# Kernel tuning notes

Hardware: AMD Instinct MI355X
Metric: run time of the kernel (lower is better)

Reference implementation:

```python
import jax, jax.numpy as jnp
import numpy as np

B = 32          # patients
D = 128         # hidden dim (modality_embedding_dim == total_hidden_dim)
H = 4           # attention heads
DH = D // H     # per-head dim
L = 2           # num_graph_layers
N = {'ct': 1024, 'pet': 1024, 'clin': 256, 'gen': 2048, 'pat': 1}
# (src_type, dst_type) for the 8 relation types registered in _setup_relations
REL = [('ct','ct'), ('pet','pet'), ('clin','clin'), ('gen','gen'),
       ('pat','clin'), ('ct','gen'), ('pet','gen'), ('gen','pat')]
E_REL = [8192, 8192, 2048, 16384, 256, 8192, 8192, 2048]
EDGE_NAMES = ['e_ct','e_pet','e_clin','e_gen','e_pat2clin','e_ct2gen','e_pet2gen','e_gen2pat']


def setup_inputs() -> dict:
    key = jax.random.key(0)
    ks = iter(jax.random.split(key, 64))
    nk = lambda: next(ks)
    inp = {}
    inp['x_ct']   = jax.random.normal(nk(), (B, N['ct'],  D), jnp.float32)
    inp['x_pet']  = jax.random.normal(nk(), (B, N['pet'], D), jnp.float32)
    inp['x_clin'] = jax.random.normal(nk(), (B, N['clin'],D), jnp.float32)
    inp['x_gen']  = jax.random.normal(nk(), (B, N['gen'], D), jnp.float32)
    inp['early']  = jax.random.normal(nk(), (B, D), jnp.float32)

    def mk_edges(k, E, ns, nd):
        k1, k2 = jax.random.split(k)
        src = jax.random.randint(k1, (B, 1, E), 0, ns, jnp.int32)
        dst = jax.random.randint(k2, (B, 1, E), 0, nd, jnp.int32)
        return jnp.concatenate([src, dst], axis=1)  # [B,2,E]

    for nm, (s, d), E in zip(EDGE_NAMES, REL, E_REL):
        inp[nm] = mk_edges(nk(), E, N[s], N[d])

    sw = 1.0 / np.sqrt(D)
    inp['W_src'] = jax.random.normal(nk(), (L, 8, D, D), jnp.float32) * sw
    inp['W_dst'] = jax.random.normal(nk(), (L, 8, D, D), jnp.float32) * sw
    inp['a_src'] = jax.random.normal(nk(), (L, 8, H, DH), jnp.float32) * sw
    inp['a_dst'] = jax.random.normal(nk(), (L, 8, H, DH), jnp.float32) * sw
    inp['Wp'] = jax.random.normal(nk(), (3, D, D), jnp.float32) * sw  # CT, PET, genomic pooling
    inp['bp'] = jnp.zeros((3, D), jnp.float32)
    inp['W_sem'] = jax.random.normal(nk(), (4 * D, 128), jnp.float32) * (1.0 / np.sqrt(4 * D))
    inp['b_sem'] = jnp.zeros((128,), jnp.float32)
    inp['q_sem'] = jax.random.normal(nk(), (128,), jnp.float32) * sw
    return inp


def _leaky_relu(x):
    return jnp.where(x > 0, x, 0.2 * x)


def _gat_layer(x, edges, Ws, Wd, As, Ad):
    """One heterogeneous multi-head GAT layer summing over relation types."""
    agg = {t: jnp.zeros((B, N[t], H, DH), jnp.float32) for t in N}
    for r, ((s, d), ei) in enumerate(zip(REL, edges)):
        hs = jnp.einsum('bnd,de->bne', x[s], Ws[r]).reshape(B, N[s], H, DH)
        hd = jnp.einsum('bnd,de->bne', x[d], Wd[r]).reshape(B, N[d], H, DH)
        al_s = jnp.sum(hs * As[r], axis=-1)  # [B,Ns,H]
        al_d = jnp.sum(hd * Ad[r], axis=-1)  # [B,Nd,H]
        nd = N[d]

        def one(hs_b, as_b, ad_b, e_b):
            src, dst = e_b[0], e_b[1]
            logit = _leaky_relu(as_b[src] + ad_b[dst])                      # [E,H]
            m = jnp.full((nd, H), -1e30, logit.dtype).at[dst].max(logit)    # segment max
            p = jnp.exp(logit - m[dst])
            den = jnp.zeros((nd, H), p.dtype).at[dst].add(p)
            w = p / (den[dst] + 1e-16)                                      # edge softmax per dst node
            msg = w[:, :, None] * hs_b[src]                                 # [E,H,DH]
            return jnp.zeros((nd, H, DH), msg.dtype).at[dst].add(msg)

        agg[d] = agg[d] + jax.vmap(one)(hs, al_s, al_d, ei)
    return {t: jax.nn.elu(agg[t].reshape(B, N[t], D)) for t in N}


def _pool(feat, W, b):
    # query = Linear(mean(features)); scores = feat @ q; softmax-weighted sum
    q = jnp.mean(feat, axis=1) @ W + b            # [B,D]
    sc = jnp.einsum('bnd,bd->bn', feat, q)        # [B,N]
    w = jax.nn.softmax(sc, axis=1)
    return jnp.einsum('bn,bnd->bd', w, feat)      # [B,D]


def _forward(x_ct, x_pet, x_clin, x_gen, early, edges,
             W_src, W_dst, a_src, a_dst, Wp, bp, W_sem, b_sem, q_sem):
    x = {'ct': x_ct, 'pet': x_pet, 'clin': x_clin, 'gen': x_gen,
         'pat': early[:, None, :]}
    for l in range(L):
        x = _gat_layer(x, edges, W_src[l], W_dst[l], a_src[l], a_dst[l])
    ct_p  = _pool(x['ct'],  Wp[0], bp[0])
    pet_p = _pool(x['pet'], Wp[1], bp[1])
    gen_p = _pool(x['gen'], Wp[2], bp[2])   # shared across the 3 meta-paths
    pad = jnp.zeros((B, 2 * D), ct_p.dtype)  # pad 2D -> 4D as in original
    imm = jnp.concatenate([ct_p, gen_p, pad], axis=1)
    pro = jnp.concatenate([pet_p, gen_p, pad], axis=1)
    trt = jnp.concatenate([(ct_p + pet_p) * 0.5, gen_p, pad], axis=1)
    z = jnp.stack([imm, pro, trt], axis=1)                     # [B,3,4D]
    s = jnp.einsum('bpa,a->bp', jnp.tanh(jnp.einsum('bpf,fa->bpa', z, W_sem) + b_sem), q_sem)
    beta = jax.nn.softmax(s, axis=1)                           # [B,3]
    fused = jnp.einsum('bp,bpf->bf', beta, z)                  # [B,4D]
    return fused, beta


def reference(x_ct, x_pet, x_clin, x_gen, early,
              e_ct, e_pet, e_clin, e_gen, e_pat2clin, e_ct2gen, e_pet2gen, e_gen2pat,
              W_src, W_dst, a_src, a_dst, Wp, bp, W_sem, b_sem, q_sem):
    edges = [e_ct, e_pet, e_clin, e_gen, e_pat2clin, e_ct2gen, e_pet2gen, e_gen2pat]
    return _forward(x_ct, x_pet, x_clin, x_gen, early, edges,
                    W_src, W_dst, a_src, a_dst, Wp, bp, W_sem, b_sem, q_sem)
```

## Files before the change

kernel.cpp:

```cpp
#include <hip/hip_runtime.h>
#include <math.h>

static constexpr int NB = 32;
static constexpr int ND = 128;

typedef short bf16x8 __attribute__((ext_vector_type(8)));
typedef float f32x4  __attribute__((ext_vector_type(4)));
typedef unsigned short u16x8 __attribute__((ext_vector_type(8)));

__device__ __forceinline__ float lrelu(float x){ return x > 0.f ? x : 0.2f*x; }
__device__ __forceinline__ unsigned short f2b(float f){
  unsigned u = __float_as_uint(f);
  return (unsigned short)((u + 0x7FFFu + ((u>>16)&1u)) >> 16);
}
__device__ __forceinline__ float b2f(unsigned short b){
  return __uint_as_float(((unsigned)b) << 16);
}

__global__ __launch_bounds__(128) void k_fold(const float* __restrict__ Wsrc,
    const float* __restrict__ Wdst, const float* __restrict__ asrc,
    const float* __restrict__ adst, float* __restrict__ vbuf){
  const int wid[5] = {0,1,3,5,6};
  int lr = blockIdx.x, role = blockIdx.y, l = blockIdx.z;
  int r = wid[lr];
  const float* W = (role ? Wdst : Wsrc) + (size_t)(l*8+r)*16384;
  const float* a = (role ? adst : asrc) + (size_t)(l*8+r)*128;
  int k = threadIdx.x;
  float* o = vbuf + ((size_t)((l*5+lr)*2+role))*512 + k*4;
  #pragma unroll
  for(int h=0;h<4;h++){
    float s = 0.f;
    #pragma unroll
    for(int j=0;j<32;j++) s += W[k*128 + h*32 + j]*a[h*32 + j];
    o[h] = s;
  }
}

__global__ __launch_bounds__(256) void k_wpack(const float* __restrict__ Wsrc,
    unsigned short* __restrict__ Wf){
  const int wid[5] = {0,1,3,5,6};
  int lr = blockIdx.x, l = blockIdx.y;
  const float* W = Wsrc + (size_t)(l*8+wid[lr])*16384;
  unsigned short* o = Wf + (size_t)((l*5+lr)*4)*4096;
  for(int idx=threadIdx.x; idx<128*128; idx+=256){
    int k = idx >> 7, col = idx & 127;
    int h = col >> 5, cc = col & 31;
    int k4 = k>>2, g = k4&3, kk = k4>>3, j = 4*((k4>>2)&1) + (k&3);
    int nb = cc>>4, lane = (cc&15) + 16*g;
    o[(size_t)h*4096 + ((size_t)((kk*2+nb)*64 + lane))*8 + j] = f2b(W[k*128 + col]);
  }
}

struct CsrP {
  const int* eg[5];
  int l2E[5];
  int Nd_[5];
  int roff_[5];
  int eoff_[5];
};

__global__ __launch_bounds__(512) void k_csr(CsrP P, int* __restrict__ rowstart,
                                             int* __restrict__ srcidx){
  int b = blockIdx.x, r = blockIdx.y, t = threadIdx.x;
  int E = 1<<P.l2E[r], Nd = P.Nd_[r];
  const int* eg = P.eg[r] + (size_t)b*2*E;
  int* rsO = rowstart + P.roff_[r] + b*(Nd+1);
  int* siO = srcidx + P.eoff_[r] + (size_t)b*E;
  __shared__ int cnt[2048];
  __shared__ int wsums[8];
  for(int i=t;i<Nd;i+=512) cnt[i]=0;
  __syncthreads();
  for(int e=t;e<E;e+=512) atomicAdd(&cnt[eg[E+e]], 1);
  __syncthreads();
  int C = Nd >> 9;
  int base = t*C;
  int loc[4]; int s_=0;
  for(int i=0;i<C;i++){ loc[i]=cnt[base+i]; s_+=loc[i]; }
  int lane = t&63, wv = t>>6;
  int sinc = s_;
  #pragma unroll
  for(int off=1;off<64;off<<=1){
    int u = __shfl_up(sinc, off);
    if(lane>=off) sinc += u;
  }
  if(lane==63) wsums[wv]=sinc;
  __syncthreads();
  int wbase=0, total=0;
  #pragma unroll
  for(int i=0;i<8;i++){ int v=wsums[i]; if(i<wv) wbase+=v; total+=v; }
  int excl = wbase + sinc - s_;
  for(int i=0;i<C;i++){
    int idx=base+i;
    rsO[idx]=excl; cnt[idx]=excl; excl+=loc[i];
  }
  if(t==0) rsO[Nd]=total;
  __syncthreads();
  for(int e=t;e<E;e+=512){
    int src=eg[e], dst=eg[E+e];
    int pos=atomicAdd(&cnt[dst],1);
    siO[pos]=src;
  }
}

struct HsP {
  int tb[4];
  int usef;
  const float* xf[3];
  unsigned long long xoff[3];
  int Ns[3];
  int nW[3];
  unsigned long long wfo[3][2];
  unsigned long long hso[3][2];
  unsigned long long aso[3][2];
  unsigned long long asrco[3][2];
  int nvd[3];
  unsigned long long vdo[3][3];
  unsigned long long aldo2[3][3];
  int ndd[3][3];
};

__global__ __launch_bounds__(256) void k_hs(HsP P, const unsigned short* __restrict__ x16,
    const unsigned short* __restrict__ Wf, const float* __restrict__ asrc,
    const float* __restrict__ vbuf, unsigned short* __restrict__ hs,
    float* __restrict__ als, float* __restrict__ ald){
  __shared__ unsigned short xl[32*132];
  __shared__ unsigned short obuf[32*136];
  int B = blockIdx.x;
  int t=0; while(t<2 && B>=P.tb[t+1]) t++;
  int local = B - P.tb[t];
  int b = local & 31, tile = local >> 5;
  int n0 = tile*32;
  int tid = threadIdx.x, w = tid>>6, ln = tid&63;
  {
    int row = tid>>3, c16 = (tid&7)*16;
    if(P.usef){
      const float* xf = P.xf[t] + ((size_t)((size_t)b*P.Ns[t] + n0 + row))*128 + c16;
      #pragma unroll
      for(int half=0; half<2; half++){
        float4 a = *(const float4*)(xf + half*8);
        float4 c = *(const float4*)(xf + half*8 + 4);
        u16x8 r;
        r[0]=f2b(a.x); r[1]=f2b(a.y); r[2]=f2b(a.z); r[3]=f2b(a.w);
        r[4]=f2b(c.x); r[5]=f2b(c.y); r[6]=f2b(c.z); r[7]=f2b(c.w);
        *(u16x8*)&xl[row*132 + c16 + half*8] = r;
      }
    } else {
      const unsigned short* xb = x16 + P.xoff[t] + ((size_t)((size_t)b*P.Ns[t] + n0 + row))*128 + c16;
      u16x8 v0 = *(const u16x8*)xb;
      u16x8 v1 = *(const u16x8*)(xb + 8);
      *(u16x8*)&xl[row*132 + c16]     = v0;
      *(u16x8*)&xl[row*132 + c16 + 8] = v1;
    }
  }
  __syncthreads();
  int g = ln>>4, r15 = ln&15;
  for(int rep=0; rep<P.nW[t]; rep++){
    const unsigned short* wf = Wf + P.wfo[t][rep] + (size_t)w*4096;
    bf16x8 bw[8];
    #pragma unroll
    for(int kk=0;kk<4;kk++){
      #pragma unroll
      for(int nb=0;nb<2;nb++)
        bw[kk*2+nb] = *(const bf16x8*)(wf + ((size_t)((kk*2+nb)*64 + ln))*8);
    }
    const float* aS = asrc + P.asrco[t][rep];
    float a0v = aS[w*32 + r15], a1v = aS[w*32 + 16 + r15];
    #pragma unroll
    for(int c=0;c<2;c++){
      f32x4 acc[2]; acc[0]=(f32x4){0,0,0,0}; acc[1]=(f32x4){0,0,0,0};
      #pragma unroll
      for(int kk=0;kk<4;kk++){
        const unsigned short* pa = &xl[(c*16 + r15)*132 + kk*32 + 4*g];
        ushort4 lo = *(const ushort4*)pa;
        ushort4 hi = *(const ushort4*)(pa+16);
        union { ushort u[8]; bf16x8 v; } tmp;
        tmp.u[0]=lo.x; tmp.u[1]=lo.y; tmp.u[2]=lo.z; tmp.u[3]=lo.w;
        tmp.u[4]=hi.x; tmp.u[5]=hi.y; tmp.u[6]=hi.z; tmp.u[7]=hi.w;
        bf16x8 af = tmp.v;
        acc[0] = __builtin_amdgcn_mfma_f32_16x16x32_bf16(af, bw[kk*2+0], acc[0], 0, 0, 0);
        acc[1] = __builtin_amdgcn_mfma_f32_16x16x32_bf16(af, bw[kk*2+1], acc[1], 0, 0, 0);
      }
      #pragma unroll
      for(int qq=0;qq<4;qq++){
        int m = c*16 + 4*g + qq;
        obuf[m*136 + w*32 + r15]      = f2b(acc[0][qq]);
        obuf[m*136 + w*32 + 16 + r15] = f2b(acc[1][qq]);
      }
      float p0 = acc[0][0]*a0v + acc[1][0]*a1v;
      float p1 = acc[0][1]*a0v + acc[1][1]*a1v;
      float p2 = acc[0][2]*a0v + acc[1][2]*a1v;
      float p3 = acc[0][3]*a0v + acc[1][3]*a1v;
      #pragma unroll
      for(int off=1; off<16; off<<=1){
        p0 += __shfl_xor(p0,off); p1 += __shfl_xor(p1,off);
        p2 += __shfl_xor(p2,off); p3 += __shfl_xor(p3,off);
      }
      if(r15 < 4){
        float pv = (r15==0)?p0:((r15==1)?p1:((r15==2)?p2:p3));
        als[P.aso[t][rep] + ((size_t)b*P.Ns[t] + n0 + c*16 + 4*g + r15)*4 + w] = pv;
      }
    }
    __syncthreads();
    {
      unsigned short* ho = hs + P.hso[t][rep] + ((size_t)b*P.Ns[t] + n0)*128;
      int row = tid>>3, c16 = (tid&7)*16;
      u16x8 o0 = *(const u16x8*)&obuf[row*136 + c16];
      u16x8 o1 = *(const u16x8*)&obuf[row*136 + c16 + 8];
      *(u16x8*)(ho + (size_t)row*128 + c16)     = o0;
      *(u16x8*)(ho + (size_t)row*128 + c16 + 8) = o1;
    }
    __syncthreads();
  }
  int nvd = P.nvd[t];
  for(int s=tid; s<(nvd<<7); s+=256){
    int vd = s>>7, rem = s&127, row = rem>>2, h = rem&3;
    const float* vv = vbuf + P.vdo[t][vd];
    float sum = 0.f;
    #pragma unroll 8
    for(int k=0;k<128;k++) sum += b2f(xl[row*132+k]) * vv[k*4+h];
    ald[P.aldo2[t][vd] + ((size_t)b*P.ndd[t][vd] + n0 + row)*4 + h] = sum;
  }
}

static constexpr int WSL = 240;

struct Fu5P {
  int nrel[3], ndshift[3];
  int roff[3][3], eoff[3][3], E[3][3], Ns[3][3];
  int rowbase[3][3];
  unsigned long long aldo[3][3];
  unsigned long long outoff[3];
};

__global__ __launch_bounds__(512, 8) void k_fuse7(Fu5P P,
    const int* __restrict__ rowstart, const int* __restrict__ srcidx,
    const float* __restrict__ als, const float* __restrict__ ald,
    const unsigned short* __restrict__ hs, unsigned short* __restrict__ out16){
  __shared__ float wlds_all[8*4*WSL];
  __shared__ int   silds_all[8*WSL];
  int B = blockIdx.x;
  int w = threadIdx.x >> 6, ln = threadIdx.x & 63;
  int xcd = B & 7, slot = B >> 3;
  int bg = slot >> 6, rem = slot & 63;
  int b = bg*8 + xcd;
  int v = rem*8 + w;
  int g = v >> 2, k4 = v & 3;
  int t, tile;
  if(k4 < 2){ t = 0; tile = g*2 + k4; }
  else if(k4 == 2){ t = 1; tile = g; }
  else { t = 2; tile = g; }
  int Nd = 1 << P.ndshift[t];
  int d0 = tile * 8;
  int nrel = P.nrel[t];
  float* wlds = wlds_all + w*4*WSL;
  int*  silds = silds_all + w*WSL;
  int dst = ln >> 3, sub = ln & 7;
  int d = d0 + dst;

  int len0=0, len1=0, len2=0, s00=0, s01=0, s02=0;
  {
    const int* rsq = rowstart + P.roff[t][0] + b*(Nd+1);
    s00 = rsq[d]; len0 = rsq[d+1] - s00;
  }
  if(nrel > 1){
    const int* rsq1 = rowstart + P.roff[t][1] + b*(Nd+1);
    s01 = rsq1[d]; len1 = rsq1[d+1] - s01;
    const int* rsq2 = rowstart + P.roff[t][2] + b*(Nd+1);
    s02 = rsq2[d]; len2 = rsq2[d+1] - s02;
  }
  int clen = len0 + len1 + len2;
  int mybase = 0;
  #pragma unroll
  for(int dd=0; dd<7; dd++){
    int vl = __shfl(clen, dd*8);
    if(dd < dst) mybase += vl;
  }

  auto dorel = [&](int q, int s0q, int lq, int segb){
    const int* si = srcidx + P.eoff[t][q] + (size_t)b*P.E[t][q] + s0q;
    int bake = P.rowbase[t][q] + b*P.Ns[t][q];
    float4 ad4 = *(const float4*)(ald + P.aldo[t][q] + ((size_t)b*Nd + d)*4);
    float dn0=0.f, dn1=0.f, dn2=0.f, dn3=0.f;
    for(int i=sub; i<lq; i+=8){
      int e = segb + i;
      int sil = bake + si[i];
      silds[e] = sil;
      float4 as4 = *(const float4*)(als + 4*(size_t)sil);
      float p0 = __expf(lrelu(as4.x+ad4.x));
      float p1 = __expf(lrelu(as4.y+ad4.y));
      float p2 = __expf(lrelu(as4.z+ad4.z));
      float p3 = __expf(lrelu(as4.w+ad4.w));
      wlds[0*WSL+e]=p0; wlds[1*WSL+e]=p1; wlds[2*WSL+e]=p2; wlds[3*WSL+e]=p3;
      dn0+=p0; dn1+=p1; dn2+=p2; dn3+=p3;
    }
    dn0+=__shfl_xor(dn0,1); dn1+=__shfl_xor(dn1,1); dn2+=__shfl_xor(dn2,1); dn3+=__shfl_xor(dn3,1);
    dn0+=__shfl_xor(dn0,2); dn1+=__shfl_xor(dn1,2); dn2+=__shfl_xor(dn2,2); dn3+=__shfl_xor(dn3,2);
    dn0+=__shfl_xor(dn0,4); dn1+=__shfl_xor(dn1,4); dn2+=__shfl_xor(dn2,4); dn3+=__shfl_xor(dn3,4);
    float i0=1.f/(dn0+1e-16f), i1=1.f/(dn1+1e-16f);
    float i2=1.f/(dn2+1e-16f), i3=1.f/(dn3+1e-16f);
    for(int i=sub; i<lq; i+=8){
      int e = segb + i;
      wlds[0*WSL+e]*=i0; wlds[1*WSL+e]*=i1;
      wlds[2*WSL+e]*=i2; wlds[3*WSL+e]*=i3;
    }
  };
  dorel(0, s00, len0, mybase);
  if(nrel > 1){
    dorel(1, s01, len1, mybase + len0);
    dorel(2, s02, len2, mybase + len0 + len1);
  }
  __builtin_amdgcn_wave_barrier();

  int h = ln>>4;
  int run = 0;
  #pragma unroll
  for(int it=0; it<8; it++){
    int cl = __shfl(clen, it*8);
    int e0 = run, e1 = run + cl; run = e1;
    float a0 = 0.f, a1 = 0.f;
    int e = e0;
    int eal = (e0+3)&~3; if(eal > e1) eal = e1;
    for(; e<eal; e++){
      float wv = wlds[h*WSL + e];
      unsigned vv = *(const unsigned*)(hs + ((size_t)silds[e]*128 + 2*ln));
      a0 += wv*__uint_as_float(vv<<16);
      a1 += wv*__uint_as_float(vv&0xFFFF0000u);
    }
    for(; e+8<=e1; e+=8){
      int4  sq0 = *(const int4*)&silds[e];
      int4  sq1 = *(const int4*)&silds[e+4];
      float4 wq0 = *(const float4*)&wlds[h*WSL + e];
      float4 wq1 = *(const float4*)&wlds[h*WSL + e + 4];
      unsigned v0 = *(const unsigned*)(hs + ((size_t)sq0.x*128 + 2*ln));
      unsigned v1 = *(const unsigned*)(hs + ((size_t)sq0.y*128 + 2*ln));
      unsigned v2 = *(const unsigned*)(hs + ((size_t)sq0.z*128 + 2*ln));
      unsigned v3 = *(const unsigned*)(hs + ((size_t)sq0.w*128 + 2*ln));
      unsigned v4 = *(const unsigned*)(hs + ((size_t)sq1.x*128 + 2*ln));
      unsigned v5 = *(const unsigned*)(hs + ((size_t)sq1.y*128 + 2*ln));
      unsigned v6 = *(const unsigned*)(hs + ((size_t)sq1.z*128 + 2*ln));
      unsigned v7 = *(const unsigned*)(hs + ((size_t)sq1.w*128 + 2*ln));
      a0 += wq0.x*__uint_as_float(v0<<16); a1 += wq0.x*__uint_as_float(v0&0xFFFF0000u);
      a0 += wq0.y*__uint_as_float(v1<<16); a1 += wq0.y*__uint_as_float(v1&0xFFFF0000u);
      a0 += wq0.z*__uint_as_float(v2<<16); a1 += wq0.z*__uint_as_float(v2&0xFFFF0000u);
      a0 += wq0.w*__uint_as_float(v3<<16); a1 += wq0.w*__uint_as_float(v3&0xFFFF0000u);
      a0 += wq1.x*__uint_as_float(v4<<16); a1 += wq1.x*__uint_as_float(v4&0xFFFF0000u);
      a0 += wq1.y*__uint_as_float(v5<<16); a1 += wq1.y*__uint_as_float(v5&0xFFFF0000u);
      a0 += wq1.z*__uint_as_float(v6<<16); a1 += wq1.z*__uint_as_float(v6&0xFFFF0000u);
      a0 += wq1.w*__uint_as_float(v7<<16); a1 += wq1.w*__uint_as_float(v7&0xFFFF0000u);
    }
    for(; e+4<=e1; e+=4){
      int4  sq = *(const int4*)&silds[e];
      float4 wq = *(const float4*)&wlds[h*WSL + e];
      unsigned v0 = *(const unsigned*)(hs + ((size_t)sq.x*128 + 2*ln));
      unsigned v1 = *(const unsigned*)(hs + ((size_t)sq.y*128 + 2*ln));
      unsigned v2 = *(const unsigned*)(hs + ((size_t)sq.z*128 + 2*ln));
      unsigned v3 = *(const unsigned*)(hs + ((size_t)sq.w*128 + 2*ln));
      a0 += wq.x*__uint_as_float(v0<<16); a1 += wq.x*__uint_as_float(v0&0xFFFF0000u);
      a0 += wq.y*__uint_as_float(v1<<16); a1 += wq.y*__uint_as_float(v1&0xFFFF0000u);
      a0 += wq.z*__uint_as_float(v2<<16); a1 += wq.z*__uint_as_float(v2&0xFFFF0000u);
      a0 += wq.w*__uint_as_float(v3<<16); a1 += wq.w*__uint_as_float(v3&0xFFFF0000u);
    }
    for(; e<e1; e++){
      float wv = wlds[h*WSL + e];
      unsigned vv = *(const unsigned*)(hs + ((size_t)silds[e]*128 + 2*ln));
      a0 += wv*__uint_as_float(vv<<16);
      a1 += wv*__uint_as_float(vv&0xFFFF0000u);
    }
    int m = d0 + it;
    float o0 = a0 > 0.f ? a0 : expm1f(a0);
    float o1 = a1 > 0.f ? a1 : expm1f(a1);
    ushort2 o; o.x = f2b(o0); o.y = f2b(o1);
    *(ushort2*)(out16 + P.outoff[t] + ((size_t)b*Nd + m)*128 + 2*ln) = o;
  }
}

__device__ __constant__ const size_t POFF[3] = {0ull, 4194304ull, 8388608ull};
__device__ __constant__ const int    PNN[3]  = {1024, 1024, 2048};
static constexpr int PCH = 64;
static constexpr int MAXCH = 32;

__global__ __launch_bounds__(128) void k_pool_psum(const unsigned short* __restrict__ x2,
    float* __restrict__ part){
  int p = blockIdx.z, b = blockIdx.x, c = blockIdx.y, t = threadIdx.x;
  int Nn = PNN[p];
  if(c*PCH >= Nn) return;
  const unsigned short* f = x2 + POFF[p] + ((size_t)b*Nn + c*PCH)*ND;
  float acc = 0.f;
  #pragma unroll 8
  for(int n=0;n<PCH;n++) acc += b2f(f[(size_t)n*ND + t]);
  part[(((size_t)p*NB + b)*MAXCH + c)*ND + t] = acc;
}

__global__ __launch_bounds__(128) void k_pool_q(const float* __restrict__ part,
    const float* __restrict__ Wp, const float* __restrict__ bp,
    float* __restrict__ q){
  int p = blockIdx.z, b = blockIdx.x, t = threadIdx.x;
  int nch = PNN[p]/PCH;
  __shared__ float mean[ND];
  float s = 0.f;
  for(int c=0;c<nch;c++) s += part[(((size_t)p*NB + b)*MAXCH + c)*ND + t];
  mean[t] = s / (float)PNN[p];
  __syncthreads();
  const float* W = Wp + (size_t)p*ND*ND;
  float qv = bp[p*ND + t];
  #pragma unroll 8
  for(int k=0;k<ND;k++) qv += mean[k]*W[k*ND + t];
  q[((size_t)p*NB + b)*ND + t] = qv;
}

__global__ __launch_bounds__(256) void k_pool_score(const unsigned short* __restrict__ x2,
    const float* __restrict__ q, float* __restrict__ sc){
  int p = blockIdx.z, b = blockIdx.y;
  int w = threadIdx.x >> 6, lane = threadIdx.x & 63;
  int n = blockIdx.x*4 + w;
  int Nn = PNN[p];
  if(n >= Nn) return;
  const unsigned short* f  = x2 + POFF[p] + ((size_t)b*Nn + n)*ND;
  const float* qb = q + ((size_t)p*NB + b)*ND;
  float s = b2f(f[lane])*qb[lane] + b2f(f[lane+64])*qb[lane+64];
  #pragma unroll
  for(int off=32; off; off>>=1) s += __shfl_xor(s, off);
  if(lane == 0) sc[((size_t)p*NB + b)*2048 + n] = s;
}

__global__ __launch_bounds__(256) void k_pool_smax(const float* __restrict__ sc,
    float* __restrict__ stat){
  int p = blockIdx.z, b = blockIdx.x, t = threadIdx.x;
  int Nn = PNN[p];
  __shared__ float red[256];
  const float* s = sc + ((size_t)p*NB + b)*2048;
  float mx = -1e30f;
  for(int n=t;n<Nn;n+=256) mx = fmaxf(mx, s[n]);
  red[t] = mx; __syncthreads();
  for(int o=128;o;o>>=1){ if(t<o) red[t]=fmaxf(red[t],red[t+o]); __syncthreads(); }
  mx = red[0]; __syncthreads();
  float sum = 0.f;
  for(int n=t;n<Nn;n+=256) sum += __expf(s[n]-mx);
  red[t] = sum; __syncthreads();
  for(int o=128;o;o>>=1){ if(t<o) red[t]+=red[t+o]; __syncthreads(); }
  if(t==0){ stat[((size_t)p*NB + b)*2] = mx; stat[((size_t)p*NB + b)*2+1] = 1.f/red[0]; }
}

__global__ __launch_bounds__(128) void k_pool_wsum(const unsigned short* __restrict__ x2,
    const float* __restrict__ sc, const float* __restrict__ stat,
    float* __restrict__ part){
  int p = blockIdx.z, b = blockIdx.x, c = blockIdx.y, t = threadIdx.x;
  int Nn = PNN[p];
  if(c*PCH >= Nn) return;
  __shared__ float wsh[PCH];
  float mx  = stat[((size_t)p*NB + b)*2];
  float inv = stat[((size_t)p*NB + b)*2+1];
  if(t < PCH) wsh[t] = __expf(sc[((size_t)p*NB + b)*2048 + c*PCH + t] - mx)*inv;
  __syncthreads();
  const unsigned short* f = x2 + POFF[p] + ((size_t)b*Nn + c*PCH)*ND;
  float acc = 0.f;
  #pragma unroll 8
  for(int n=0;n<PCH;n++) acc += wsh[n]*b2f(f[(size_t)n*ND + t]);
  part[(((size_t)p*NB + b)*MAXCH + c)*ND + t] = acc;
}

__global__ __launch_bounds__(128) void k_pool_comb(const float* __restrict__ part,
    float* __restrict__ pooled){
  int p = blockIdx.z, b = blockIdx.x, t = threadIdx.x;
  int nch = PNN[p]/PCH;
  float s = 0.f;
  for(int c=0;c<nch;c++) s += part[(((size_t)p*NB + b)*MAXCH + c)*ND + t];
  pooled[((size_t)p*NB + b)*ND + t] = s;
}

__global__ __launch_bounds__(128) void k_sem(const float* __restrict__ ctp,
    const float* __restrict__ petp, const float* __restrict__ genp,
    const float* __restrict__ Wsem, const float* __restrict__ bsem,
    const float* __restrict__ qsem, float* __restrict__ fused, float* __restrict__ beta){
  int b = blockIdx.x, t = threadIdx.x;
  __shared__ float z[3][256];
  __shared__ float red[128];
  float ct = ctp[b*ND + t], pet = petp[b*ND + t], gen = genp[b*ND + t];
  z[0][t]=ct;  z[1][t]=pet; z[2][t]=0.5f*(ct+pet);
  z[0][ND+t]=gen; z[1][ND+t]=gen; z[2][ND+t]=gen;
  __syncthreads();
  float s[3];
  for(int p=0;p<3;p++){
    float a = bsem[t];
    for(int f=0;f<256;f++) a += z[p][f]*Wsem[f*128 + t];
    a = tanhf(a);
    red[t] = a * qsem[t];
    __syncthreads();
    for(int o=64;o>0;o>>=1){ if(t<o) red[t]+=red[t+o]; __syncthreads(); }
    s[p] = red[0]; __syncthreads();
  }
  float mx = fmaxf(s[0], fmaxf(s[1], s[2]));
  float e0 = __expf(s[0]-mx), e1 = __expf(s[1]-mx), e2 = __expf(s[2]-mx);
  float sm = e0+e1+e2;
  float b0 = e0/sm, b1 = e1/sm, b2 = e2/sm;
  if(t < 3) beta[b*3 + t] = (t==0)?b0:((t==1)?b1:b2);
  float f0 = b0*z[0][t] + b1*z[1][t] + b2*z[2][t];
  float f1 = b0*z[0][ND+t] + b1*z[1][ND+t] + b2*z[2][ND+t];
  fused[(size_t)b*512 + t]       = f0;
  fused[(size_t)b*512 + 128 + t] = f1;
  fused[(size_t)b*512 + 256 + t] = 0.f;
  fused[(size_t)b*512 + 384 + t] = 0.f;
}

extern "C" void kernel_launch(void* const* d_in, const int* in_sizes, int n_in,
                              void* d_out, int out_size, void* d_ws, size_t ws_size,
                              hipStream_t stream) {
  static const int wid[5]    = {0,1,3,5,6};
  static const int edgein[5] = {5,6,8,10,11};
  static const int l2E[5]    = {13,13,14,13,13};
  static const int Nd_l[5]   = {1024,1024,2048,2048,2048};
  static const int E_l[5]    = {8192,8192,16384,8192,8192};
  static const int Ns_l[5]   = {1024,1024,2048,1024,1024};
  static const int eoff[6]   = {0,262144,524288,1048576,1310720,1572864};
  static const int roff[5]   = {0,32800,65600,131168,196736};
  static const unsigned long long aoff[5]   = {0,131072,262144,524288,655360};
  static const unsigned long long aldoff[5] = {0,131072,262144,524288,786432};
  static const unsigned long long hsoff_lr[5] = {0ull,4194304ull,8388608ull,16777216ull,20971520ull};
  static const unsigned long long ALD = 786432;

  const float* Wsrc = (const float*)d_in[13];
  const float* Wp   = (const float*)d_in[17];
  const float* bp   = (const float*)d_in[18];
  const float* Wsem = (const float*)d_in[19];
  const float* bsem = (const float*)d_in[20];
  const float* qsem = (const float*)d_in[21];

  unsigned short* xc16 = (unsigned short*)d_ws;
  unsigned short* x2b16 = xc16;
  unsigned short* xmid16 = xc16 + 16777216;
  float* albase = (float*)(xmid16 + 16777216);
  float* als = albase;
  float* ald = albase + ALD;
  float* vbuf = albase + 1835008;
  unsigned short* wfbuf = (unsigned short*)(vbuf + 10240);
  float* pooled = (float*)(wfbuf + 163840);
  float* part = pooled + 12288;
  float* qbuf = part + 393216;
  float* scbuf = qbuf + 12288;
  float* stat = scbuf + 196608;
  int* rowstart = (int*)(stat + 192);
  int* srcidx = rowstart + 262304;
  unsigned short* hs16 = (unsigned short*)(srcidx + 1572864);

  { dim3 g(5,2,2); k_fold<<<g,128,0,stream>>>(Wsrc, (const float*)d_in[14],
                                              (const float*)d_in[15], (const float*)d_in[16], vbuf); }
  { dim3 g(5,2); k_wpack<<<g,256,0,stream>>>(Wsrc, wfbuf); }

  CsrP csr;
  for(int r=0;r<5;r++){
    csr.eg[r] = (const int*)d_in[edgein[r]];
    csr.l2E[r] = l2E[r]; csr.Nd_[r] = Nd_l[r];
    csr.roff_[r] = roff[r]; csr.eoff_[r] = eoff[r];
  }
  { dim3 g(NB,5); k_csr<<<g,512,0,stream>>>(csr, rowstart, srcidx); }

  static const unsigned long long xoo[3] = {0,4194304,8388608};
  static const int t2_nrel[3] = {3,1,1};
  static const int t2_lrel[3][3] = {{2,3,4},{0,0,0},{1,0,0}};
  static const int t2_nds[3] = {11,10,10};
  static const int t2_out[3] = {2,0,1};

  Fu5P fp;
  for(int t=0;t<3;t++){
    fp.nrel[t]=t2_nrel[t]; fp.ndshift[t]=t2_nds[t]; fp.outoff[t]=xoo[t2_out[t]];
    for(int q=0;q<3;q++){
      int lr = t2_lrel[t][q];
      fp.roff[t][q]=roff[lr]; fp.eoff[t][q]=eoff[lr];
      fp.E[t][q]=E_l[lr]; fp.Ns[t][q]=Ns_l[lr];
      fp.rowbase[t][q]=(int)(aoff[lr]/4);
      fp.aldo[t][q]=aldoff[lr];
    }
  }

  static const int hs_lr[3][2] = {{0,3},{1,4},{2,2}};
  static const int vd_lr[3][3] = {{0,0,0},{1,0,0},{2,3,4}};
  HsP hp;
  hp.tb[0]=0; hp.tb[1]=1024; hp.tb[2]=2048; hp.tb[3]=4096;
  hp.xf[0]=(const float*)d_in[0]; hp.xf[1]=(const float*)d_in[1]; hp.xf[2]=(const float*)d_in[3];
  hp.xoff[0]=0; hp.xoff[1]=4194304; hp.xoff[2]=8388608;
  hp.Ns[0]=1024; hp.Ns[1]=1024; hp.Ns[2]=2048;
  hp.nW[0]=2; hp.nW[1]=2; hp.nW[2]=1;
  hp.nvd[0]=1; hp.nvd[1]=1; hp.nvd[2]=3;
  for(int t=0;t<3;t++){
    for(int rep=0;rep<2;rep++){
      int lr = hs_lr[t][rep];
      hp.hso[t][rep]=hsoff_lr[lr];
      hp.aso[t][rep]=aoff[lr];
    }
    for(int vd=0;vd<3;vd++){
      int lr = vd_lr[t][vd];
      hp.aldo2[t][vd]=aldoff[lr];
      hp.ndd[t][vd]=Nd_l[lr];
    }
  }
  hp.hso[2][1]=0; hp.aso[2][1]=0;

  for(int l=0;l<2;l++){
    unsigned short* xout = (l==0) ? xmid16 : x2b16;
    hp.usef = (l==0) ? 1 : 0;

    for(int t=0;t<3;t++){
      for(int rep=0;rep<2;rep++){
        int lr = hs_lr[t][rep];
        hp.wfo[t][rep]=(unsigned long long)((l*5 + lr)*4)*4096;
        hp.asrco[t][rep]=(unsigned long long)((l*8 + wid[lr])*128);
      }
      for(int vd=0;vd<3;vd++){
        int lr = vd_lr[t][vd];
        hp.vdo[t][vd]=((unsigned long long)((l*5+lr)*2+1))*512;
      }
    }
    k_hs<<<4096,256,0,stream>>>(hp, xmid16, wfbuf, (const float*)d_in[15], vbuf,
                                hs16, als, ald);

    k_fuse7<<<2048,512,0,stream>>>(fp, rowstart, srcidx, als, ald, hs16, xout);
  }

  {
    dim3 gchunk(NB, MAXCH, 3);
    dim3 gone(NB, 1, 3);
    dim3 gscore(512, NB, 3);
    k_pool_psum <<<gchunk,128,0,stream>>>(x2b16, part);
    k_pool_q    <<<gone,  128,0,stream>>>(part, Wp, bp, qbuf);
    k_pool_score<<<gscore,256,0,stream>>>(x2b16, qbuf, scbuf);
    k_pool_smax <<<gone,  256,0,stream>>>(scbuf, stat);
    k_pool_wsum <<<gchunk,128,0,stream>>>(x2b16, scbuf, stat, part);
    k_pool_comb <<<gone,  128,0,stream>>>(part, pooled);
  }

  float* fused = (float*)d_out;
  float* beta  = fused + (size_t)NB*512;
  k_sem<<<NB,128,0,stream>>>(pooled, pooled + NB*ND, pooled + 2*NB*ND,
                             Wsem, bsem, qsem, fused, beta);
}
```

Baseline: 325.8 us.

## Widen fuse gather to 8-byte loads split across half-waves, prefetch weights in k_hs

The edge-aggregation kernel now has each half-wave handle alternate edges with 8-byte (4 bf16) loads per lane. It unrolls 16 edges per step and combines the two halves with a cross-lane shuffle. This is meant to raise memory-level parallelism and cut per-edge load instruction count in the gather. k_hs now preloads the next relation's packed weights before the store barrier, and the dst-attention dot product uses a transposed fold buffer so loads are vectorised. The cost is more registers, half the lanes sitting idle for the output write, and a new workspace region for the transposed buffer.

```diff
diff --git a/kernel.cpp b/kernel.cpp
--- a/kernel.cpp
+++ b/kernel.cpp
@@ -19,7 +19,8 @@
 
 __global__ __launch_bounds__(128) void k_fold(const float* __restrict__ Wsrc,
     const float* __restrict__ Wdst, const float* __restrict__ asrc,
-    const float* __restrict__ adst, float* __restrict__ vbuf){
+    const float* __restrict__ adst, float* __restrict__ vbuf,
+    float* __restrict__ vbufT){
   const int wid[5] = {0,1,3,5,6};
   int lr = blockIdx.x, role = blockIdx.y, l = blockIdx.z;
   int r = wid[lr];
@@ -33,6 +34,7 @@
     #pragma unroll
     for(int j=0;j<32;j++) s += W[k*128 + h*32 + j]*a[h*32 + j];
     o[h] = s;
+    if(role==1) vbufT[(size_t)(l*5+lr)*512 + h*128 + k] = s;
   }
 }
 
@@ -121,7 +123,7 @@
 
 __global__ __launch_bounds__(256) void k_hs(HsP P, const unsigned short* __restrict__ x16,
     const unsigned short* __restrict__ Wf, const float* __restrict__ asrc,
-    const float* __restrict__ vbuf, unsigned short* __restrict__ hs,
+    const float* __restrict__ vbufT, unsigned short* __restrict__ hs,
     float* __restrict__ als, float* __restrict__ ald){
   __shared__ unsigned short xl[32*132];
   __shared__ unsigned short obuf[32*136];
@@ -131,6 +133,12 @@
   int b = local & 31, tile = local >> 5;
   int n0 = tile*32;
   int tid = threadIdx.x, w = tid>>6, ln = tid&63;
+  bf16x8 bw[8];
+  {
+    const unsigned short* wf0 = Wf + P.wfo[t][0] + (size_t)w*4096;
+    #pragma unroll
+    for(int i=0;i<8;i++) bw[i] = *(const bf16x8*)(wf0 + ((size_t)(i*64 + ln))*8);
+  }
   {
     int row = tid>>3, c16 = (tid&7)*16;
     if(P.usef){
@@ -154,15 +162,8 @@
   }
   __syncthreads();
   int g = ln>>4, r15 = ln&15;
-  for(int rep=0; rep<P.nW[t]; rep++){
-    const unsigned short* wf = Wf + P.wfo[t][rep] + (size_t)w*4096;
-    bf16x8 bw[8];
-    #pragma unroll
-    for(int kk=0;kk<4;kk++){
-      #pragma unroll
-      for(int nb=0;nb<2;nb++)
-        bw[kk*2+nb] = *(const bf16x8*)(wf + ((size_t)((kk*2+nb)*64 + ln))*8);
-    }
+  int nW = P.nW[t];
+  for(int rep=0; rep<nW; rep++){
     const float* aS = asrc + P.asrco[t][rep];
     float a0v = aS[w*32 + r15], a1v = aS[w*32 + 16 + r15];
     #pragma unroll
@@ -200,24 +201,50 @@
         als[P.aso[t][rep] + ((size_t)b*P.Ns[t] + n0 + c*16 + 4*g + r15)*4 + w] = pv;
       }
     }
-    __syncthreads();
-    {
-      unsigned short* ho = hs + P.hso[t][rep] + ((size_t)b*P.Ns[t] + n0)*128;
-      int row = tid>>3, c16 = (tid&7)*16;
-      u16x8 o0 = *(const u16x8*)&obuf[row*136 + c16];
-      u16x8 o1 = *(const u16x8*)&obuf[row*136 + c16 + 8];
-      *(u16x8*)(ho + (size_t)row*128 + c16)     = o0;
-      *(u16x8*)(ho + (size_t)row*128 + c16 + 8) = o1;
-    }
-    __syncthreads();
+    if(rep+1 < nW){
+      const unsigned short* wfn = Wf + P.wfo[t][rep+1] + (size_t)w*4096;
+      bf16x8 bn[8];
+      #pragma unroll
+      for(int i=0;i<8;i++) bn[i] = *(const bf16x8*)(wfn + ((size_t)(i*64 + ln))*8);
+      __syncthreads();
+      {
+        unsigned short* ho = hs + P.hso[t][rep] + ((size_t)b*P.Ns[t] + n0)*128;
+        int row = tid>>3, c16 = (tid&7)*16;
+        u16x8 o0 = *(const u16x8*)&obuf[row*136 + c16];
+        u16x8 o1 = *(const u16x8*)&obuf[row*136 + c16 + 8];
+        *(u16x8*)(ho + (size_t)row*128 + c16)     = o0;
+        *(u16x8*)(ho + (size_t)row*128 + c16 + 8) = o1;
+      }
+      __syncthreads();
+      #pragma unroll
+      for(int i=0;i<8;i++) bw[i] = bn[i];
+    } else {
+      __syncthreads();
+      {
+        unsigned short* ho = hs + P.hso[t][rep] + ((size_t)b*P.Ns[t] + n0)*128;
+        int row = tid>>3, c16 = (tid&7)*16;
+        u16x8 o0 = *(const u16x8*)&obuf[row*136 + c16];
+        u16x8 o1 = *(const u16x8*)&obuf[row*136 + c16 + 8];
+        *(u16x8*)(ho + (size_t)row*128 + c16)     = o0;
+        *(u16x8*)(ho + (size_t)row*128 + c16 + 8) = o1;
+      }
+    }
   }
   int nvd = P.nvd[t];
   for(int s=tid; s<(nvd<<7); s+=256){
     int vd = s>>7, rem = s&127, row = rem>>2, h = rem&3;
-    const float* vv = vbuf + P.vdo[t][vd];
+    const float* vT = vbufT + P.vdo[t][vd] + h*128;
     float sum = 0.f;
-    #pragma unroll 8
-    for(int k=0;k<128;k++) sum += b2f(xl[row*132+k]) * vv[k*4+h];
+    #pragma unroll 4
+    for(int k8=0;k8<128;k8+=8){
+      u16x8 xv = *(const u16x8*)&xl[row*132 + k8];
+      float4 va = *(const float4*)(vT + k8);
+      float4 vb = *(const float4*)(vT + k8 + 4);
+      sum += b2f((unsigned short)xv[0])*va.x + b2f((unsigned short)xv[1])*va.y
+           + b2f((unsigned short)xv[2])*va.z + b2f((unsigned short)xv[3])*va.w
+           + b2f((unsigned short)xv[4])*vb.x + b2f((unsigned short)xv[5])*vb.y
+           + b2f((unsigned short)xv[6])*vb.z + b2f((unsigned short)xv[7])*vb.w;
+    }
     ald[P.aldo2[t][vd] + ((size_t)b*P.ndd[t][vd] + n0 + row)*4 + h] = sum;
   }
 }
@@ -232,7 +259,15 @@
   unsigned long long outoff[3];
 };
 
-__global__ __launch_bounds__(512, 8) void k_fuse7(Fu5P P,
+#define GLD2(k) \
+  int o##k = silds[e+2*k+eh]; \
+  float w##k = wlds[hsel*WSL + e+2*k+eh]; \
+  uint2 v##k = *(const uint2*)(hsc + (((size_t)(unsigned)o##k)<<8) + lnoff);
+#define ACC2(k) \
+  a0 += w##k*__uint_as_float(v##k.x<<16); a1 += w##k*__uint_as_float(v##k.x&0xFFFF0000u); \
+  a2 += w##k*__uint_as_float(v##k.y<<16); a3 += w##k*__uint_as_float(v##k.y&0xFFFF0000u);
+
+__global__ __launch_bounds__(512, 8) void k_fuse8(Fu5P P,
     const int* __restrict__ rowstart, const int* __restrict__ srcidx,
     const float* __restrict__ als, const float* __restrict__ ald,
     const unsigned short* __restrict__ hs, unsigned short* __restrict__ out16){
@@ -311,66 +346,43 @@
   }
   __builtin_amdgcn_wave_barrier();
 
-  int h = ln>>4;
+  int li = ln & 31, eh = ln >> 5;
+  size_t lnoff = (size_t)(li*8);
+  int hsel = li >> 3;
+  const char* hsc = (const char*)hs;
   int run = 0;
   #pragma unroll
   for(int it=0; it<8; it++){
     int cl = __shfl(clen, it*8);
     int e0 = run, e1 = run + cl; run = e1;
-    float a0 = 0.f, a1 = 0.f;
+    float a0=0.f, a1=0.f, a2=0.f, a3=0.f;
     int e = e0;
-    int eal = (e0+3)&~3; if(eal > e1) eal = e1;
-    for(; e<eal; e++){
-      float wv = wlds[h*WSL + e];
-      unsigned vv = *(const unsigned*)(hs + ((size_t)silds[e]*128 + 2*ln));
-      a0 += wv*__uint_as_float(vv<<16);
-      a1 += wv*__uint_as_float(vv&0xFFFF0000u);
-    }
-    for(; e+8<=e1; e+=8){
-      int4  sq0 = *(const int4*)&silds[e];
-      int4  sq1 = *(const int4*)&silds[e+4];
-      float4 wq0 = *(const float4*)&wlds[h*WSL + e];
-      float4 wq1 = *(const float4*)&wlds[h*WSL + e + 4];
-      unsigned v0 = *(const unsigned*)(hs + ((size_t)sq0.x*128 + 2*ln));
-      unsigned v1 = *(const unsigned*)(hs + ((size_t)sq0.y*128 + 2*ln));
-      unsigned v2 = *(const unsigned*)(hs + ((size_t)sq0.z*128 + 2*ln));
-      unsigned v3 = *(const unsigned*)(hs + ((size_t)sq0.w*128 + 2*ln));
-      unsigned v4 = *(const unsigned*)(hs + ((size_t)sq1.x*128 + 2*ln));
-      unsigned v5 = *(const unsigned*)(hs + ((size_t)sq1.y*128 + 2*ln));
-      unsigned v6 = *(const unsigned*)(hs + ((size_t)sq1.z*128 + 2*ln));
-      unsigned v7 = *(const unsigned*)(hs + ((size_t)sq1.w*128 + 2*ln));
-      a0 += wq0.x*__uint_as_float(v0<<16); a1 += wq0.x*__uint_as_float(v0&0xFFFF0000u);
-      a0 += wq0.y*__uint_as_float(v1<<16); a1 += wq0.y*__uint_as_float(v1&0xFFFF0000u);
-      a0 += wq0.z*__uint_as_float(v2<<16); a1 += wq0.z*__uint_as_float(v2&0xFFFF0000u);
-      a0 += wq0.w*__uint_as_float(v3<<16); a1 += wq0.w*__uint_as_float(v3&0xFFFF0000u);
-      a0 += wq1.x*__uint_as_float(v4<<16); a1 += wq1.x*__uint_as_float(v4&0xFFFF0000u);
-      a0 += wq1.y*__uint_as_float(v5<<16); a1 += wq1.y*__uint_as_float(v5&0xFFFF0000u);
-      a0 += wq1.z*__uint_as_float(v6<<16); a1 += wq1.z*__uint_as_float(v6&0xFFFF0000u);
-      a0 += wq1.w*__uint_as_float(v7<<16); a1 += wq1.w*__uint_as_float(v7&0xFFFF0000u);
-    }
-    for(; e+4<=e1; e+=4){
-      int4  sq = *(const int4*)&silds[e];
-      float4 wq = *(const float4*)&wlds[h*WSL + e];
-      unsigned v0 = *(const unsigned*)(hs + ((size_t)sq.x*128 + 2*ln));
-      unsigned v1 = *(const unsigned*)(hs + ((size_t)sq.y*128 + 2*ln));
-      unsigned v2 = *(const unsigned*)(hs + ((size_t)sq.z*128 + 2*ln));
-      unsigned v3 = *(const unsigned*)(hs + ((size_t)sq.w*128 + 2*ln));
-      a0 += wq.x*__uint_as_float(v0<<16); a1 += wq.x*__uint_as_float(v0&0xFFFF0000u);
-      a0 += wq.y*__uint_as_float(v1<<16); a1 += wq.y*__uint_as_float(v1&0xFFFF0000u);
-      a0 += wq.z*__uint_as_float(v2<<16); a1 += wq.z*__uint_as_float(v2&0xFFFF0000u);
-      a0 += wq.w*__uint_as_float(v3<<16); a1 += wq.w*__uint_as_float(v3&0xFFFF0000u);
-    }
-    for(; e<e1; e++){
-      float wv = wlds[h*WSL + e];
-      unsigned vv = *(const unsigned*)(hs + ((size_t)silds[e]*128 + 2*ln));
-      a0 += wv*__uint_as_float(vv<<16);
-      a1 += wv*__uint_as_float(vv&0xFFFF0000u);
-    }
-    int m = d0 + it;
-    float o0 = a0 > 0.f ? a0 : expm1f(a0);
-    float o1 = a1 > 0.f ? a1 : expm1f(a1);
-    ushort2 o; o.x = f2b(o0); o.y = f2b(o1);
-    *(ushort2*)(out16 + P.outoff[t] + ((size_t)b*Nd + m)*128 + 2*ln) = o;
+    for(; e+16<=e1; e+=16){
+      GLD2(0) GLD2(1) GLD2(2) GLD2(3) GLD2(4) GLD2(5) GLD2(6) GLD2(7)
+      ACC2(0) ACC2(1) ACC2(2) ACC2(3) ACC2(4) ACC2(5) ACC2(6) ACC2(7)
+    }
+    for(; e<e1; e+=2){
+      int idx = e + eh;
+      bool val = idx < e1;
+      int idx2 = val ? idx : e;
+      int o = silds[idx2];
+      float wraw = wlds[hsel*WSL + idx2];
+      float wv = val ? wraw : 0.f;
+      uint2 vv = *(const uint2*)(hsc + (((size_t)(unsigned)o)<<8) + lnoff);
+      a0 += wv*__uint_as_float(vv.x<<16); a1 += wv*__uint_as_float(vv.x&0xFFFF0000u);
+      a2 += wv*__uint_as_float(vv.y<<16); a3 += wv*__uint_as_float(vv.y&0xFFFF0000u);
+    }
+    a0 += __shfl_xor(a0,32); a1 += __shfl_xor(a1,32);
+    a2 += __shfl_xor(a2,32); a3 += __shfl_xor(a3,32);
+    if(eh == 0){
+      int m = d0 + it;
+      a0 = a0 > 0.f ? a0 : expm1f(a0);
+      a1 = a1 > 0.f ? a1 : expm1f(a1);
+      a2 = a2 > 0.f ? a2 : expm1f(a2);
+      a3 = a3 > 0.f ? a3 : expm1f(a3);
+      ushort4 o4; o4.x=f2b(a0); o4.y=f2b(a1); o4.z=f2b(a2); o4.w=f2b(a3);
+      *(ushort4*)(out16 + P.outoff[t] + ((size_t)b*Nd + m)*128 + li*4) = o4;
+    }
   }
 }
 
@@ -541,9 +553,11 @@
   int* rowstart = (int*)(stat + 192);
   int* srcidx = rowstart + 262304;
   unsigned short* hs16 = (unsigned short*)(srcidx + 1572864);
+  float* vbufT = (float*)(hs16 + 25165824);
 
   { dim3 g(5,2,2); k_fold<<<g,128,0,stream>>>(Wsrc, (const float*)d_in[14],
-                                              (const float*)d_in[15], (const float*)d_in[16], vbuf); }
+                                              (const float*)d_in[15], (const float*)d_in[16],
+                                              vbuf, vbufT); }
   { dim3 g(5,2); k_wpack<<<g,256,0,stream>>>(Wsrc, wfbuf); }
 
   CsrP csr;
@@ -607,13 +621,13 @@
       }
       for(int vd=0;vd<3;vd++){
         int lr = vd_lr[t][vd];
-        hp.vdo[t][vd]=((unsigned long long)((l*5+lr)*2+1))*512;
-      }
-    }
-    k_hs<<<4096,256,0,stream>>>(hp, xmid16, wfbuf, (const float*)d_in[15], vbuf,
+        hp.vdo[t][vd]=(unsigned long long)((l*5+lr)*512);
+      }
+    }
+    k_hs<<<4096,256,0,stream>>>(hp, xmid16, wfbuf, (const float*)d_in[15], vbufT,
                                 hs16, als, ald);
 
-    k_fuse7<<<2048,512,0,stream>>>(fp, rowstart, srcidx, als, ald, hs16, xout);
+    k_fuse8<<<2048,512,0,stream>>>(fp, rowstart, srcidx, als, ald, hs16, xout);
   }
 
   {
```

Measured after the change: 449.1 us. 37.9% more time.
